# Performance work log

Measured on AMD Instinct MI355X. Metric: run time of the kernel, lower is better.

The kernel has to match this reference:

```python
import jax, jax.numpy as jnp
import numpy as np
import math

B, CIN, CH, H, W = 4, 64, 32, 64, 64
M_CH, DEPTH, K = 4, 3, 8
NPF = CIN // 2  # num_pos_feats per axis; pos channels = 2*NPF = CIN
TEMPERATURE = 10000.0


def sine_pos(h, w, npf, temperature=TEMPERATURE):
    # PositionEmbeddingSine with normalize=False; cumsum of ones == arange(1, n+1)
    y_embed = jnp.arange(1, h + 1, dtype=jnp.float32)
    x_embed = jnp.arange(1, w + 1, dtype=jnp.float32)
    dim_t = jnp.arange(npf, dtype=jnp.float32)
    dim_t = temperature ** (2.0 * jnp.floor(dim_t / 2.0) / npf)
    pos_x = jnp.broadcast_to(x_embed[None, :, None] / dim_t, (h, w, npf))
    pos_y = jnp.broadcast_to(y_embed[:, None, None] / dim_t, (h, w, npf))

    def interleave(p):
        return jnp.stack([jnp.sin(p[..., 0::2]), jnp.cos(p[..., 1::2])], axis=-1).reshape(h, w, npf)

    pos = jnp.concatenate([interleave(pos_y), interleave(pos_x)], axis=-1)  # (h,w,2*npf)
    return jnp.transpose(pos, (2, 0, 1))  # (2*npf, h, w)


def conv2d(x, wgt, bias, pad):
    y = jax.lax.conv_general_dilated(
        x, wgt, window_strides=(1, 1), padding=[(pad, pad), (pad, pad)],
        dimension_numbers=('NCHW', 'OIHW', 'NCHW'))
    return y + bias[None, :, None, None]


def setup_inputs() -> dict:
    key = jax.random.key(0)
    ks = jax.random.split(key, 13)
    s = 0.05
    return {
        'f':    jax.random.normal(ks[0], (B, CH, H, W), jnp.float32),
        'map':  jax.random.normal(ks[1], (B, 1, 32, 32), jnp.float32),
        'f_q':  jax.random.normal(ks[2], (B, CIN, H, W), jnp.float32),
        'f_k':  jax.random.normal(ks[3], (B, CIN, H, W), jnp.float32),
        'm_k':  jax.random.normal(ks[4], (B, 1, 32, 32), jnp.float32),
        'wq':   jax.random.normal(ks[5], (M_CH, CIN), jnp.float32) * s,
        'wk':   jax.random.normal(ks[6], (M_CH, CIN), jnp.float32) * s,
        'w_in':  jax.random.normal(ks[7], (CH, CH, 1, 1), jnp.float32) * s,
        'b_in':  jax.random.normal(ks[8], (CH,), jnp.float32) * s,
        'w_mid': jax.random.normal(ks[9], (DEPTH, CH, CH, 3, 3), jnp.float32) * s,
        'b_mid': jax.random.normal(ks[10], (DEPTH, CH), jnp.float32) * s,
        'w_out': jax.random.normal(ks[11], (1, CH, 3, 3), jnp.float32) * s,
        'b_out': jax.random.normal(ks[12], (1,), jnp.float32) * s,
    }


def reference(f, map, f_q, f_k, m_k, wq, wk, w_in, b_in, w_mid, b_mid, w_out, b_out):
    b, c, h, w = f_q.shape
    hf, wf = f.shape[2], f.shape[3]
    # self.ret: bilinear resize to f's spatial size (align_corners=False)
    map_r = jax.image.resize(map, (b, 1, hf, wf), method='bilinear')
    m_k_r = jax.image.resize(m_k, (b, 1, hf, wf), method='bilinear')

    pos = sine_pos(h, w, NPF)[None]  # (1, CIN, h, w); same for pos_emb_h/pos_emb_l
    fq_emb = f_q + pos
    fk_emb = f_k + pos

    # 1x1 convs == channel matmuls
    query = jnp.einsum('mc,bchw->bhwm', wq, fq_emb).reshape(b, h * w, M_CH)  # (b, N, m)
    key_t = jnp.einsum('mc,bchw->bmhw', wk, fk_emb).reshape(b, M_CH, h * w)  # (b, m, N)

    sim = jnp.einsum('bqm,bmk->bqk', query, key_t)   # (b, N, N)
    sim = jax.nn.softmax(sim, axis=-2)                # softmax over query axis (dim=-2)

    value = (jnp.exp(m_k_r) / math.e).reshape(b, 1, h * w)  # broadcast over query axis
    context = sim * value
    context_k, _ = jax.lax.top_k(context, K)          # (b, N, K) over last (key) axis
    context_m = jnp.mean(context_k, axis=-1)          # (b, N)
    corrected_map = context_m.reshape(b, 1, h, w)

    corrected_map = corrected_map * map_r + map_r
    rmap = 1.0 - jax.nn.sigmoid(corrected_map)

    x = rmap * f  # broadcast over channel dim
    x = conv2d(x, w_in, b_in, 0)
    for i in range(DEPTH):
        x = jax.nn.relu(conv2d(x, w_mid[i], b_mid[i], 1))
    out = conv2d(x, w_out, b_out, 1) + corrected_map
    return (x, out, corrected_map)
```

## Files before the change

### kernel.cpp

```cpp
#include <hip/hip_runtime.h>
#include <hip/hip_bf16.h>
#include <math.h>

#define BB 4
#define CIN 64
#define CH 32
#define HH 64
#define WW 64
#define NN 4096
#define MCH 4
#define NQCH 32
#define LOG2E 1.4426950408889634f

#define PP_OFF     0
#define Q4_OFF     1024
#define K4_OFF     66560
#define CV_OFF     132096
#define CPSUM_OFF  672768
#define RMAP_OFF   148480
#define CMAPF_OFF  164864
#define T8_OFF     181248
#define XA_OFF     181248
#define XB_OFF     705536

#define OUT_X_OFF   0
#define OUT_O_OFF   524288
#define OUT_CM_OFF  540672

__device__ __forceinline__ float bilin32(const float* src, int b, int y, int x) {
    float sy = 0.5f * y - 0.25f;
    float sx = 0.5f * x - 0.25f;
    float fy0 = floorf(sy), fx0 = floorf(sx);
    int y0 = (int)fy0, x0 = (int)fx0;
    float fy = sy - fy0, fx = sx - fx0;
    int y0c = min(max(y0, 0), 31), y1c = min(max(y0 + 1, 0), 31);
    int x0c = min(max(x0, 0), 31), x1c = min(max(x0 + 1, 0), 31);
    const float* p = src + b * 1024;
    float v00 = p[y0c * 32 + x0c], v01 = p[y0c * 32 + x1c];
    float v10 = p[y1c * 32 + x0c], v11 = p[y1c * 32 + x1c];
    float v0 = v00 + fx * (v01 - v00);
    float v1 = v10 + fx * (v11 - v10);
    return v0 + fy * (v1 - v0);
}

__global__ void k0_posproj(const float* __restrict__ wq, const float* __restrict__ wk,
                           float* __restrict__ pp) {
    int t = threadIdx.x;
    float coord = (float)(t + 1);
    float qy[4] = {0,0,0,0}, qx[4] = {0,0,0,0}, ky[4] = {0,0,0,0}, kx[4] = {0,0,0,0};
    for (int c = 0; c < 32; ++c) {
        float e = (2.0f * (float)(c / 2)) / 32.0f;
        float dim = powf(10000.0f, e);
        float ang = coord / dim;
        float pr = (c & 1) ? cosf(ang) : sinf(ang);
        #pragma unroll
        for (int m = 0; m < 4; ++m) {
            qy[m] += wq[m * 64 + c] * pr;
            qx[m] += wq[m * 64 + 32 + c] * pr;
            ky[m] += wk[m * 64 + c] * pr;
            kx[m] += wk[m * 64 + 32 + c] * pr;
        }
    }
    #pragma unroll
    for (int m = 0; m < 4; ++m) {
        pp[0 * 256 + m * 64 + t] = qy[m];
        pp[1 * 256 + m * 64 + t] = qx[m];
        pp[2 * 256 + m * 64 + t] = ky[m];
        pp[3 * 256 + m * 64 + t] = kx[m];
    }
}

__global__ void k1_qk(const float* __restrict__ fq, const float* __restrict__ fk,
                      const float* __restrict__ wq, const float* __restrict__ wk,
                      const float* __restrict__ pp,
                      float* __restrict__ Q4, float* __restrict__ K4) {
    __shared__ float wqs[256], wks[256];
    __shared__ float red[256][9];
    int tid = threadIdx.x;
    wqs[tid] = wq[tid];
    wks[tid] = wk[tid];
    __syncthreads();
    int qi = tid & 63, g = tid >> 6;
    int gid = blockIdx.x * 64 + qi;
    int b = gid >> 12, hw = gid & 4095;
    const float* fqb = fq + (size_t)b * CIN * NN + hw;
    const float* fkb = fk + (size_t)b * CIN * NN + hw;
    float aq[4] = {0,0,0,0}, ak[4] = {0,0,0,0};
    int c0 = g * 16;
    #pragma unroll 4
    for (int c = c0; c < c0 + 16; ++c) {
        float vq = fqb[c * NN];
        float vk = fkb[c * NN];
        #pragma unroll
        for (int m = 0; m < 4; ++m) {
            aq[m] += wqs[m * 64 + c] * vq;
            ak[m] += wks[m * 64 + c] * vk;
        }
    }
    #pragma unroll
    for (int m = 0; m < 4; ++m) { red[tid][m] = aq[m]; red[tid][4 + m] = ak[m]; }
    __syncthreads();
    if (tid < 64) {
        int y = hw >> 6, x = hw & 63;
        float q4[4], k4[4];
        #pragma unroll
        for (int m = 0; m < 4; ++m) {
            q4[m] = LOG2E * (red[tid][m] + red[tid + 64][m] + red[tid + 128][m] + red[tid + 192][m]
                  + pp[0 * 256 + m * 64 + y] + pp[1 * 256 + m * 64 + x]);
            k4[m] = red[tid][4 + m] + red[tid + 64][4 + m] + red[tid + 128][4 + m] + red[tid + 192][4 + m]
                  + pp[2 * 256 + m * 64 + y] + pp[3 * 256 + m * 64 + x];
        }
        ((float4*)Q4)[gid] = make_float4(q4[0], q4[1], q4[2], q4[3]);
        ((float4*)K4)[gid] = make_float4(k4[0], k4[1], k4[2], k4[3]);
    }
}

__global__ void k2a_colstats(const float* __restrict__ Q4, const float* __restrict__ K4,
                             float* __restrict__ cpsum) {
    __shared__ float4 Qs[128];
    int blk = blockIdx.x;
    int kblk = blk & 7;   blk >>= 3;
    int qch  = blk & 31;  blk >>= 5;
    int b    = blk;
    int tid = threadIdx.x;
    if (tid < 128)
        Qs[tid] = ((const float4*)Q4)[b * NN + qch * 128 + tid];
    __syncthreads();
    int k0 = kblk * 512 + tid;
    float4 kva = ((const float4*)K4)[b * NN + k0];
    float4 kvb = ((const float4*)K4)[b * NN + k0 + 256];
    float sa = 0.0f, sb = 0.0f;
    #pragma unroll 8
    for (int i = 0; i < 128; ++i) {
        float4 q = Qs[i];
        float da = fmaf(q.x, kva.x, fmaf(q.y, kva.y, fmaf(q.z, kva.z, q.w * kva.w)));
        float db = fmaf(q.x, kvb.x, fmaf(q.y, kvb.y, fmaf(q.z, kvb.z, q.w * kvb.w)));
        sa += exp2f(da);
        sb += exp2f(db);
    }
    cpsum[(b * NQCH + qch) * NN + k0] = sa;
    cpsum[(b * NQCH + qch) * NN + k0 + 256] = sb;
}

__global__ void k2b_cmerge(const float* __restrict__ cpsum,
                           const float* __restrict__ m_k, float* __restrict__ cvals) {
    int gid = blockIdx.x * 256 + threadIdx.x;
    int b = gid >> 12, k = gid & 4095;
    float S = 0.0f;
    #pragma unroll
    for (int j = 0; j < NQCH; ++j) S += cpsum[(b * NQCH + j) * NN + k];
    float mk = bilin32(m_k, b, k >> 6, k & 63);
    cvals[gid] = LOG2E * (mk - 1.0f) - log2f(S);
}

__global__ void k3a_scan(const float* __restrict__ Q4, const float* __restrict__ K4,
                         const float* __restrict__ cvals, float* __restrict__ t8) {
    __shared__ float4 kvs[512];
    __shared__ float  cvs[512];
    int blk = blockIdx.x;
    int kc = blk & 7;   blk >>= 3;
    int g2 = blk & 15;  blk >>= 4;
    int b  = blk;
    int tid = threadIdx.x;
    int wave = tid >> 6, lane = tid & 63;

    const float4* Kb = (const float4*)K4 + b * NN + kc * 512;
    const float* cb = cvals + b * NN + kc * 512;
    #pragma unroll
    for (int i = tid; i < 512; i += 256) {
        kvs[i] = Kb[i];
        cvs[i] = cb[i];
    }
    __syncthreads();

    int qrow = (g2 * 4 + wave) * 64 + lane;
    float4 qv = ((const float4*)Q4)[b * NN + qrow];
    float t0 = -1e30f, t1 = -1e30f, t2 = -1e30f, t3 = -1e30f;
    float t4 = -1e30f, t5 = -1e30f, t6 = -1e30f, t7 = -1e30f;
    #pragma unroll 4
    for (int i = 0; i < 512; ++i) {
        float4 kv = kvs[i];
        float s = fmaf(qv.x, kv.x, fmaf(qv.y, kv.y,
                  fmaf(qv.z, kv.z, fmaf(qv.w, kv.w, cvs[i]))));
        if (s > t0) {
            float a = fmaxf(t0, s);
            t0 = fminf(a, t1); a = fmaxf(a, t1);
            t1 = fminf(a, t2); a = fmaxf(a, t2);
            t2 = fminf(a, t3); a = fmaxf(a, t3);
            t3 = fminf(a, t4); a = fmaxf(a, t4);
            t4 = fminf(a, t5); a = fmaxf(a, t5);
            t5 = fminf(a, t6); a = fmaxf(a, t6);
            t6 = fminf(a, t7); t7 = fmaxf(a, t7);
        }
    }
    float* o = t8 + ((size_t)(b * NN + qrow)) * 64 + kc * 8;
    o[0] = t0; o[1] = t1; o[2] = t2; o[3] = t3;
    o[4] = t4; o[5] = t5; o[6] = t6; o[7] = t7;
}

__global__ void k3b_merge(const float* __restrict__ t8, const float* __restrict__ mapin,
                          float* __restrict__ rmap, float* __restrict__ cmapf,
                          float* __restrict__ outp) {
    int tid = threadIdx.x;
    int qid = blockIdx.x * 4 + (tid >> 6);
    int lane = tid & 63;
    float v = t8[(size_t)qid * 64 + lane];
    float sm = 0.0f;
    #pragma unroll
    for (int r = 0; r < 8; ++r) {
        float m = v;
        int ln = lane;
        #pragma unroll
        for (int off = 32; off >= 1; off >>= 1) {
            float om = __shfl_xor(m, off);
            int ol = __shfl_xor(ln, off);
            if (om > m || (om == m && ol < ln)) { m = om; ln = ol; }
        }
        sm += exp2f(m);
        if (lane == ln) v = -1e30f;
    }
    if (lane == 0) {
        float cmv = sm * 0.125f;
        int b = qid >> 12, hw = qid & 4095;
        float mr = bilin32(mapin, b, hw >> 6, hw & 63);
        float cm = cmv * mr + mr;
        float rm = 1.0f / (1.0f + __expf(cm));
        rmap[qid] = rm;
        cmapf[qid] = cm;
        outp[OUT_CM_OFF + qid] = cm;
    }
}

__global__ void k4_conv1(const float* __restrict__ f, const float* __restrict__ rmap,
                         const float* __restrict__ w_in, const float* __restrict__ b_in,
                         float* __restrict__ xout) {
    __shared__ float ws_[1024];
    __shared__ float bs[32];
    int tid = threadIdx.x;
    for (int i = tid; i < 1024; i += 256) ws_[i] = w_in[i];
    if (tid < 32) bs[tid] = b_in[tid];
    __syncthreads();
    int gid = blockIdx.x * 256 + tid;
    int hw = gid & 4095;
    int og = (gid >> 12) & 7;
    int b  = gid >> 15;
    float rm = rmap[b * NN + hw];
    float acc[4];
    #pragma unroll
    for (int j = 0; j < 4; ++j) acc[j] = bs[og * 4 + j];
    const float* fb = f + (size_t)b * CH * NN + hw;
    for (int i = 0; i < 32; ++i) {
        float v = fb[i * NN] * rm;
        #pragma unroll
        for (int j = 0; j < 4; ++j) acc[j] += ws_[(og * 4 + j) * 32 + i] * v;
    }
    float* xo = xout + (size_t)b * CH * NN + (og * 4) * NN + hw;
    #pragma unroll
    for (int j = 0; j < 4; ++j) xo[j * NN] = acc[j];
}

__global__ void k5_conv3(const float* __restrict__ xin, const float* __restrict__ w,
                         const float* __restrict__ bias, float* __restrict__ xout,
                         float* __restrict__ outx) {
    __shared__ float tile[32][324];
    __shared__ float wsm[1152];
    __shared__ float bsm[4];
    int blk = blockIdx.x;
    int og = blk & 7;  blk >>= 3;
    int tx = blk & 3;  blk >>= 2;
    int ty = blk & 3;  blk >>= 2;
    int b  = blk;
    int tid = threadIdx.x;
    for (int i = tid; i < 1152; i += 256) wsm[i] = w[og * 1152 + i];
    if (tid < 4) bsm[tid] = bias[og * 4 + tid];
    int y0 = ty * 16 - 1, x0 = tx * 16 - 1;
    for (int i = tid; i < 32 * 324; i += 256) {
        int c = i / 324, r = i % 324;
        int yy = r / 18, xx = r % 18;
        int gy = y0 + yy, gx = x0 + xx;
        float v = 0.0f;
        if (gy >= 0 && gy < 64 && gx >= 0 && gx < 64)
            v = xin[((size_t)b * CH + c) * NN + gy * 64 + gx];
        tile[c][r] = v;
    }
    __syncthreads();
    int py = tid >> 4, px = tid & 15;
    float acc[4];
    #pragma unroll
    for (int j = 0; j < 4; ++j) acc[j] = bsm[j];
    for (int i = 0; i < 32; ++i) {
        const float* tr = &tile[i][py * 18 + px];
        float v00 = tr[0],  v01 = tr[1],  v02 = tr[2];
        float v10 = tr[18], v11 = tr[19], v12 = tr[20];
        float v20 = tr[36], v21 = tr[37], v22 = tr[38];
        #pragma unroll
        for (int j = 0; j < 4; ++j) {
            const float* wj = &wsm[j * 288 + i * 9];
            acc[j] += v00 * wj[0] + v01 * wj[1] + v02 * wj[2]
                    + v10 * wj[3] + v11 * wj[4] + v12 * wj[5]
                    + v20 * wj[6] + v21 * wj[7] + v22 * wj[8];
        }
    }
    size_t base = (size_t)b * CH * NN + (size_t)(og * 4) * NN
                + (ty * 16 + py) * 64 + tx * 16 + px;
    #pragma unroll
    for (int j = 0; j < 4; ++j) {
        float r_ = fmaxf(acc[j], 0.0f);
        xout[base + j * NN] = r_;
        if (outx) outx[base + j * NN] = r_;
    }
}

__global__ void k6_convout(const float* __restrict__ xin, const float* __restrict__ w_out,
                           const float* __restrict__ b_out, const float* __restrict__ cmapf,
                           float* __restrict__ outp) {
    __shared__ float wsm[288];
    __shared__ float red[256];
    int tid = threadIdx.x;
    for (int i = tid; i < 288; i += 256) wsm[i] = w_out[i];
    int pxi = tid & 63, g = tid >> 6;
    int gid = blockIdx.x * 64 + pxi;
    int b = gid >> 12, hw = gid & 4095;
    int y = hw >> 6, x = hw & 63;
    __syncthreads();
    float acc = 0.0f;
    int c0 = g * 8;
    for (int i = c0; i < c0 + 8; ++i) {
        const float* xi = xin + ((size_t)b * CH + i) * NN;
        #pragma unroll
        for (int ky = 0; ky < 3; ++ky) {
            int gy = y + ky - 1;
            if (gy < 0 || gy > 63) continue;
            #pragma unroll
            for (int kx = 0; kx < 3; ++kx) {
                int gx = x + kx - 1;
                if (gx < 0 || gx > 63) continue;
                acc += xi[gy * 64 + gx] * wsm[i * 9 + ky * 3 + kx];
            }
        }
    }
    red[tid] = acc;
    __syncthreads();
    if (tid < 64) {
        float a = red[tid] + red[tid + 64] + red[tid + 128] + red[tid + 192]
                + b_out[0] + cmapf[gid];
        outp[OUT_O_OFF + gid] = a;
    }
}

extern "C" void kernel_launch(void* const* d_in, const int* in_sizes, int n_in,
                              void* d_out, int out_size, void* d_ws, size_t ws_size,
                              hipStream_t stream) {
    const float* f     = (const float*)d_in[0];
    const float* mapin = (const float*)d_in[1];
    const float* f_q   = (const float*)d_in[2];
    const float* f_k   = (const float*)d_in[3];
    const float* m_k   = (const float*)d_in[4];
    const float* wq    = (const float*)d_in[5];
    const float* wk    = (const float*)d_in[6];
    const float* w_in  = (const float*)d_in[7];
    const float* b_in  = (const float*)d_in[8];
    const float* w_mid = (const float*)d_in[9];
    const float* b_mid = (const float*)d_in[10];
    const float* w_out = (const float*)d_in[11];
    const float* b_out = (const float*)d_in[12];
    float* outp = (float*)d_out;
    float* ws = (float*)d_ws;

    float* PP    = ws + PP_OFF;
    float* Q4    = ws + Q4_OFF;
    float* K4    = ws + K4_OFF;
    float* CV    = ws + CV_OFF;
    float* CPSUM = ws + CPSUM_OFF;
    float* RMAP  = ws + RMAP_OFF;
    float* CMAPF = ws + CMAPF_OFF;
    float* T8    = ws + T8_OFF;
    float* XA    = ws + XA_OFF;
    float* XB    = ws + XB_OFF;

    k0_posproj<<<1, 64, 0, stream>>>(wq, wk, PP);
    k1_qk<<<256, 256, 0, stream>>>(f_q, f_k, wq, wk, PP, Q4, K4);
    k2a_colstats<<<BB * NQCH * 8, 256, 0, stream>>>(Q4, K4, CPSUM);
    k2b_cmerge<<<64, 256, 0, stream>>>(CPSUM, m_k, CV);
    k3a_scan<<<BB * 16 * 8, 256, 0, stream>>>(Q4, K4, CV, T8);
    k3b_merge<<<BB * NN / 4, 256, 0, stream>>>(T8, mapin, RMAP, CMAPF, outp);
    k4_conv1<<<512, 256, 0, stream>>>(f, RMAP, w_in, b_in, XA);
    k5_conv3<<<512, 256, 0, stream>>>(XA, w_mid + 0 * 9216, b_mid + 0 * 32, XB, (float*)0);
    k5_conv3<<<512, 256, 0, stream>>>(XB, w_mid + 1 * 9216, b_mid + 1 * 32, XA, (float*)0);
    k5_conv3<<<512, 256, 0, stream>>>(XA, w_mid + 2 * 9216, b_mid + 2 * 32, XB, outp + OUT_X_OFF);
    k6_convout<<<256, 256, 0, stream>>>(XB, w_out, b_out, CMAPF, outp);
}
```

Measured before the change: 235.5 us.

## Split top-8 key scan across two wave halves with dual independent chains

The top-8 scan kernel now runs 512 threads per block. Each query row is handled by two waves, each covering half of the 512-key chunk, and each wave keeps two independent top-8 lists so the running insertion chains interleave. The partial lists are merged with bitonic compare-exchange steps, and the upper half passes its result to the lower half through shared memory. This targets the serial dependency of the insertion sort and the low occupancy of the 512-block launch, at the cost of an extra barrier, shared-memory traffic and more registers.

```diff
diff --git a/kernel.cpp b/kernel.cpp
--- a/kernel.cpp
+++ b/kernel.cpp
@@ -26,6 +26,8 @@
 #define OUT_X_OFF   0
 #define OUT_O_OFF   524288
 #define OUT_CM_OFF  540672
+
+#define CE(x, y) { float ce_lo = fminf(x, y); y = fmaxf(x, y); x = ce_lo; }
 
 __device__ __forceinline__ float bilin32(const float* src, int b, int y, int x) {
     float sy = 0.5f * y - 0.25f;
@@ -153,49 +155,86 @@
     cvals[gid] = LOG2E * (mk - 1.0f) - log2f(S);
 }
 
-__global__ void k3a_scan(const float* __restrict__ Q4, const float* __restrict__ K4,
-                         const float* __restrict__ cvals, float* __restrict__ t8) {
+__global__ __launch_bounds__(512) void k3a_scan(
+        const float* __restrict__ Q4, const float* __restrict__ K4,
+        const float* __restrict__ cvals, float* __restrict__ t8) {
     __shared__ float4 kvs[512];
     __shared__ float  cvs[512];
+    __shared__ float  sbuf[4][64][9];
     int blk = blockIdx.x;
     int kc = blk & 7;   blk >>= 3;
     int g2 = blk & 15;  blk >>= 4;
     int b  = blk;
     int tid = threadIdx.x;
     int wave = tid >> 6, lane = tid & 63;
+    int half = wave >> 2, wsub = wave & 3;
 
     const float4* Kb = (const float4*)K4 + b * NN + kc * 512;
     const float* cb = cvals + b * NN + kc * 512;
-    #pragma unroll
-    for (int i = tid; i < 512; i += 256) {
-        kvs[i] = Kb[i];
-        cvs[i] = cb[i];
-    }
-    __syncthreads();
-
-    int qrow = (g2 * 4 + wave) * 64 + lane;
+    if (tid < 512) { kvs[tid] = Kb[tid]; cvs[tid] = cb[tid]; }
+    __syncthreads();
+
+    int qrow = (g2 * 4 + wsub) * 64 + lane;
     float4 qv = ((const float4*)Q4)[b * NN + qrow];
-    float t0 = -1e30f, t1 = -1e30f, t2 = -1e30f, t3 = -1e30f;
-    float t4 = -1e30f, t5 = -1e30f, t6 = -1e30f, t7 = -1e30f;
-    #pragma unroll 4
-    for (int i = 0; i < 512; ++i) {
-        float4 kv = kvs[i];
-        float s = fmaf(qv.x, kv.x, fmaf(qv.y, kv.y,
-                  fmaf(qv.z, kv.z, fmaf(qv.w, kv.w, cvs[i]))));
-        if (s > t0) {
-            float a = fmaxf(t0, s);
-            t0 = fminf(a, t1); a = fmaxf(a, t1);
-            t1 = fminf(a, t2); a = fmaxf(a, t2);
-            t2 = fminf(a, t3); a = fmaxf(a, t3);
-            t3 = fminf(a, t4); a = fmaxf(a, t4);
-            t4 = fminf(a, t5); a = fmaxf(a, t5);
-            t5 = fminf(a, t6); a = fmaxf(a, t6);
-            t6 = fminf(a, t7); t7 = fmaxf(a, t7);
-        }
-    }
-    float* o = t8 + ((size_t)(b * NN + qrow)) * 64 + kc * 8;
-    o[0] = t0; o[1] = t1; o[2] = t2; o[3] = t3;
-    o[4] = t4; o[5] = t5; o[6] = t6; o[7] = t7;
+
+    float a0=-1e30f,a1=-1e30f,a2=-1e30f,a3=-1e30f,a4=-1e30f,a5=-1e30f,a6=-1e30f,a7=-1e30f;
+    float c0=-1e30f,c1=-1e30f,c2=-1e30f,c3=-1e30f,c4=-1e30f,c5=-1e30f,c6=-1e30f,c7=-1e30f;
+    int base = half * 256;
+    #pragma unroll 2
+    for (int i = 0; i < 128; ++i) {
+        float4 ka = kvs[base + i];
+        float sa = fmaf(qv.x, ka.x, fmaf(qv.y, ka.y,
+                   fmaf(qv.z, ka.z, fmaf(qv.w, ka.w, cvs[base + i]))));
+        float4 kb = kvs[base + 128 + i];
+        float sb = fmaf(qv.x, kb.x, fmaf(qv.y, kb.y,
+                   fmaf(qv.z, kb.z, fmaf(qv.w, kb.w, cvs[base + 128 + i]))));
+        if (sa > a0) {
+            float z = fmaxf(a0, sa);
+            a0 = fminf(z, a1); z = fmaxf(z, a1);
+            a1 = fminf(z, a2); z = fmaxf(z, a2);
+            a2 = fminf(z, a3); z = fmaxf(z, a3);
+            a3 = fminf(z, a4); z = fmaxf(z, a4);
+            a4 = fminf(z, a5); z = fmaxf(z, a5);
+            a5 = fminf(z, a6); z = fmaxf(z, a6);
+            a6 = fminf(z, a7); a7 = fmaxf(z, a7);
+        }
+        if (sb > c0) {
+            float z = fmaxf(c0, sb);
+            c0 = fminf(z, c1); z = fmaxf(z, c1);
+            c1 = fminf(z, c2); z = fmaxf(z, c2);
+            c2 = fminf(z, c3); z = fmaxf(z, c3);
+            c3 = fminf(z, c4); z = fmaxf(z, c4);
+            c4 = fminf(z, c5); z = fmaxf(z, c5);
+            c5 = fminf(z, c6); z = fmaxf(z, c6);
+            c6 = fminf(z, c7); c7 = fmaxf(z, c7);
+        }
+    }
+    float r0 = fmaxf(a0, c7), r1 = fmaxf(a1, c6), r2 = fmaxf(a2, c5), r3 = fmaxf(a3, c4);
+    float r4 = fmaxf(a4, c3), r5 = fmaxf(a5, c2), r6 = fmaxf(a6, c1), r7 = fmaxf(a7, c0);
+    CE(r0, r4); CE(r1, r5); CE(r2, r6); CE(r3, r7);
+    CE(r0, r2); CE(r1, r3); CE(r4, r6); CE(r5, r7);
+    CE(r0, r1); CE(r2, r3); CE(r4, r5); CE(r6, r7);
+
+    if (half == 1) {
+        float* sb_ = &sbuf[wsub][lane][0];
+        sb_[0] = r0; sb_[1] = r1; sb_[2] = r2; sb_[3] = r3;
+        sb_[4] = r4; sb_[5] = r5; sb_[6] = r6; sb_[7] = r7;
+    }
+    __syncthreads();
+    if (half == 0) {
+        const float* sb_ = &sbuf[wsub][lane][0];
+        float f0 = fmaxf(r0, sb_[7]);
+        float f1 = fmaxf(r1, sb_[6]);
+        float f2 = fmaxf(r2, sb_[5]);
+        float f3 = fmaxf(r3, sb_[4]);
+        float f4 = fmaxf(r4, sb_[3]);
+        float f5 = fmaxf(r5, sb_[2]);
+        float f6 = fmaxf(r6, sb_[1]);
+        float f7 = fmaxf(r7, sb_[0]);
+        float* o = t8 + ((size_t)(b * NN + qrow)) * 64 + kc * 8;
+        o[0] = f0; o[1] = f1; o[2] = f2; o[3] = f3;
+        o[4] = f4; o[5] = f5; o[6] = f6; o[7] = f7;
+    }
 }
 
 __global__ void k3b_merge(const float* __restrict__ t8, const float* __restrict__ mapin,
@@ -382,7 +421,7 @@
     k1_qk<<<256, 256, 0, stream>>>(f_q, f_k, wq, wk, PP, Q4, K4);
     k2a_colstats<<<BB * NQCH * 8, 256, 0, stream>>>(Q4, K4, CPSUM);
     k2b_cmerge<<<64, 256, 0, stream>>>(CPSUM, m_k, CV);
-    k3a_scan<<<BB * 16 * 8, 256, 0, stream>>>(Q4, K4, CV, T8);
+    k3a_scan<<<BB * 16 * 8, 512, 0, stream>>>(Q4, K4, CV, T8);
     k3b_merge<<<BB * NN / 4, 256, 0, stream>>>(T8, mapin, RMAP, CMAPF, outp);
     k4_conv1<<<512, 256, 0, stream>>>(f, RMAP, w_in, b_in, XA);
     k5_conv3<<<512, 256, 0, stream>>>(XA, w_mid + 0 * 9216, b_mid + 0 * 32, XB, (float*)0);
```

After: 229.3 us. -2.6%, faster.
